# Optimization experiments

Hardware: AMD Instinct MI355X
Metric: run time of the kernel (lower is better)

The kernel has to match this reference:

```python
import jax, jax.numpy as jnp
import numpy as np

NUM_HEADS = 12
EPS = 1e-12  # torch F.normalize clamp_min eps


def _l2norm(t):
    return t / jnp.clip(jnp.linalg.norm(t, axis=-1, keepdims=True), EPS)


def setup_inputs() -> dict:
    key = jax.random.key(0)
    ks = jax.random.split(key, 6)
    B, N, C = 8, 4096, 768
    Nc, Nb, F = 1, 512, 16
    s = 0.02
    return {
        "x": jax.random.normal(ks[0], (B, N, C), jnp.float32),
        "bank": jax.random.normal(ks[1], (Nc, Nb, F), jnp.float32),
        "Wq": jax.random.normal(ks[2], (C, C), jnp.float32) * s,
        "Wkv": jax.random.normal(ks[3], (F, 2 * C), jnp.float32) * s,
        "Wlin": jax.random.normal(ks[4], (C, C), jnp.float32) * s,
        "b_lin": jnp.zeros((C,), jnp.float32),
        "prelu_a": jnp.asarray(0.25, jnp.float32),
        "temperature": jnp.ones((NUM_HEADS, 1, 1), jnp.float32),
    }


def reference(x, bank, Wq, Wkv, Wlin, b_lin, prelu_a, temperature):
    B, N, C = x.shape
    Nc, Nb, _ = bank.shape
    H = NUM_HEADS
    d = C // H
    # q: (B, H, N, d), L2-normalized along d
    q = _l2norm((x @ Wq).reshape(B, N, H, d).transpose(0, 2, 1, 3))
    # kv from (detached) bank: (2, Nc, H, Nb, d)
    kv = (bank @ Wkv).reshape(Nc, Nb, 2, H, d).transpose(2, 0, 3, 1, 4)
    k = _l2norm(kv[0])
    v = kv[1]
    # cosine attention with per-head learned temperature: (B, Nc, H, N, Nb)
    attn = jnp.einsum('bhnd,chmd->bchnm', q, k) * temperature
    attn = jax.nn.softmax(attn, axis=-1)
    # (dropout is identity in eval mode)
    out = jnp.einsum('bchnm,chmd->bchnd', attn, v)  # (B, Nc, H, N, d)
    out = out.reshape(B * Nc, H, N, d).transpose(0, 2, 1, 3).reshape(B, N, C)
    out = out @ Wlin + b_lin
    # PReLU with a single shared parameter
    return jnp.where(out >= 0, out, prelu_a * out)
```

## Files before the change

kernel.cpp:

```cpp
#include <hip/hip_runtime.h>
#include <cstdint>
#include <cstddef>

typedef unsigned short u16;
typedef __attribute__((ext_vector_type(8))) __bf16 bf16x8;
typedef __attribute__((ext_vector_type(4))) float f32x4;

#define MFMA(a, b, c) __builtin_amdgcn_mfma_f32_16x16x32_bf16(a, b, c, 0, 0, 0)

__device__ __forceinline__ u16 f2bf(float f) {
  union { float f; uint32_t u; } x; x.f = f;
  uint32_t r = x.u + 0x7fffu + ((x.u >> 16) & 1u);
  return (u16)(r >> 16);
}

__device__ __forceinline__ void gld16(const u16* g, u16* l) {
  __builtin_amdgcn_global_load_lds(
      (const __attribute__((address_space(1))) void*)g,
      (__attribute__((address_space(3))) void*)l, 16, 0, 0);
}

__global__ void cvt_f32_bf16(const float* __restrict__ src, u16* __restrict__ dst, int n4) {
  int i = blockIdx.x * blockDim.x + threadIdx.x;
  int stride = gridDim.x * blockDim.x;
  for (; i < n4; i += stride) {
    float4 v = ((const float4*)src)[i];
    ushort4 o;
    o.x = f2bf(v.x); o.y = f2bf(v.y); o.z = f2bf(v.z); o.w = f2bf(v.w);
    ((ushort4*)dst)[i] = o;
  }
}

__global__ void prep_kern(const float* __restrict__ Wq, u16* __restrict__ wqt,
                          const float* __restrict__ Wlin, u16* __restrict__ wlt,
                          const float* __restrict__ bank, const float* __restrict__ Wkv,
                          const float* __restrict__ temp, u16* __restrict__ Kb,
                          u16* __restrict__ VT) {
  const int b = blockIdx.x;
  if (b < 1152) {
    __shared__ float tile[32][33];
    const float* src = (b >= 576) ? Wlin : Wq;
    u16* dst = (b >= 576) ? wlt : wqt;
    const int r = (b >= 576) ? b - 576 : b;
    const int bx = (r % 24) * 32, by = (r / 24) * 32;
    const int tx = threadIdx.x & 31, ty = threadIdx.x >> 5;
    #pragma unroll
    for (int i = ty; i < 32; i += 8)
      tile[i][tx] = src[(size_t)(by + i) * 768 + bx + tx];
    __syncthreads();
    #pragma unroll
    for (int i = ty; i < 32; i += 8)
      dst[(size_t)(bx + i) * 768 + by + tx] = f2bf(tile[tx][i]);
  } else {
    const int bb = b - 1152;
    const int h = bb >> 7;
    const int m = ((bb & 127) << 2) + (threadIdx.x >> 6);
    const int j = threadIdx.x & 63;
    const float* br = bank + m * 16;
    float kj = 0.f, vj = 0.f;
    #pragma unroll
    for (int f = 0; f < 16; ++f) {
      float bv = br[f];
      kj = fmaf(bv, Wkv[f * 1536 + h * 64 + j], kj);
      vj = fmaf(bv, Wkv[f * 1536 + 768 + h * 64 + j], vj);
    }
    float ss = kj * kj;
    #pragma unroll
    for (int o = 32; o; o >>= 1) ss += __shfl_xor(ss, o);
    float rn = rsqrtf(fmaxf(ss, 1e-24f));
    Kb[((size_t)h * 512 + m) * 64 + j] = f2bf(kj * rn * temp[h] * 1.4426950408889634f);
    VT[((size_t)h * 64 + j) * 512 + m] = f2bf(vj);
  }
}

template <int MODE>
__global__ __launch_bounds__(256, 3) void gemm_bt(
    const u16* __restrict__ A, const u16* __restrict__ BT, void* __restrict__ Cout,
    int M, int N, int K, const float* __restrict__ bias, const float* __restrict__ prelu) {
  __shared__ u16 sA[3][128 * 32];
  __shared__ u16 sB[3][128 * 32];
  const int ntiles = N >> 7;
  const int swz = (blockIdx.x & 7) * (gridDim.x >> 3) + (blockIdx.x >> 3);
  const int m0 = (swz / ntiles) << 7;
  const int n0 = (swz % ntiles) << 7;
  const int tid = threadIdx.x;
  const int w = tid >> 6, lane = tid & 63;
  const int wm = (w >> 1) << 6, wn = (w & 1) << 6;
  const int srow = lane >> 2, scol = (lane & 3) << 3;
  const u16* ga = A + (size_t)(m0 + (w << 5) + srow) * K + scol;
  const u16* gb = BT + (size_t)(n0 + (w << 5) + srow) * K + scol;
  const int lofs = (w << 5) * 32;
  const int fr = lane & 15, fq = (lane >> 4) << 3;
  f32x4 acc[4][4] = {};

  auto stage = [&](int buf, int k0) {
    gld16(ga + k0, sA[buf] + lofs);
    gld16(ga + k0 + (size_t)16 * K, sA[buf] + lofs + 16 * 32);
    gld16(gb + k0, sB[buf] + lofs);
    gld16(gb + k0 + (size_t)16 * K, sB[buf] + lofs + 16 * 32);
  };

  const int nk = K >> 5;
  stage(0, 0);
  stage(1, 32);
  int cb = 0;
  int sb = 2;
  for (int it = 0; it < nk; ++it) {
    asm volatile("s_waitcnt vmcnt(4)\n\ts_barrier" ::: "memory");
    int nx = it + 2; if (nx >= nk) nx -= nk;
    stage(sb, nx << 5);
    bf16x8 af[4], bfr[4];
    #pragma unroll
    for (int t = 0; t < 4; ++t) {
      af[t] = *(const bf16x8*)(sA[cb] + (wm + t * 16 + fr) * 32 + fq);
      bfr[t] = *(const bf16x8*)(sB[cb] + (wn + t * 16 + fr) * 32 + fq);
    }
    #pragma unroll
    for (int i = 0; i < 4; ++i)
      #pragma unroll
      for (int j = 0; j < 4; ++j)
        acc[i][j] = MFMA(af[i], bfr[j], acc[i][j]);
    cb = (cb == 2) ? 0 : cb + 1;
    sb = (sb == 2) ? 0 : sb + 1;
  }

  const int q = lane >> 4;
  float a = (MODE == 1) ? prelu[0] : 0.f;
  #pragma unroll
  for (int tm = 0; tm < 4; ++tm)
    #pragma unroll
    for (int tn = 0; tn < 4; ++tn) {
      int col = n0 + wn + tn * 16 + fr;
      float bv = (MODE == 1) ? bias[col] : 0.f;
      #pragma unroll
      for (int r = 0; r < 4; ++r) {
        int row = m0 + wm + tm * 16 + q * 4 + r;
        float v = acc[tm][tn][r];
        if (MODE == 1) {
          v += bv;
          v = v >= 0.f ? v : v * a;
          ((float*)Cout)[(size_t)row * N + col] = v;
        } else {
          ((u16*)Cout)[(size_t)row * N + col] = f2bf(v);
        }
      }
    }
}

__global__ __launch_bounds__(512, 4) void attn_kern(
    const u16* __restrict__ Q, const u16* __restrict__ Kb,
    const u16* __restrict__ Vt, u16* __restrict__ O) {
  __shared__ __align__(16) u16 sK[2][64 * 72];
  __shared__ __align__(16) u16 sV[2][64 * 72];

  const int qb = blockIdx.x & 127;
  const int h = blockIdx.x >> 7;
  const int tid = threadIdx.x, w = tid >> 6, lane = tid & 63;
  const int fr = lane & 15, quad = lane >> 4;
  const int rowbase = qb * 256 + (w << 5);

  bf16x8 qa[2][2];
  #pragma unroll
  for (int g = 0; g < 2; ++g) {
    const u16* qp = Q + (size_t)(rowbase + g * 16 + fr) * 768 + h * 64 + (quad << 3);
    qa[g][0] = *(const bf16x8*)qp;
    qa[g][1] = *(const bf16x8*)(qp + 32);
    float ss = 0.f;
    #pragma unroll
    for (int j = 0; j < 8; ++j) {
      float f0 = (float)qa[g][0][j], f1 = (float)qa[g][1][j];
      ss += f0 * f0 + f1 * f1;
    }
    ss += __shfl_xor(ss, 16);
    ss += __shfl_xor(ss, 32);
    float rn = rsqrtf(fmaxf(ss, 1e-24f));
    #pragma unroll
    for (int j = 0; j < 8; ++j) {
      qa[g][0][j] = (__bf16)((float)qa[g][0][j] * rn);
      qa[g][1][j] = (__bf16)((float)qa[g][1][j] * rn);
    }
  }

  const u16* kg = Kb + (size_t)h * 512 * 64;
  const u16* vg = Vt + (size_t)h * 64 * 512;
  int4 kreg, vreg;
  auto load_chunk = [&](int c) {
    kreg = *(const int4*)(kg + (size_t)(c * 64 + (tid >> 3)) * 64 + (tid & 7) * 8);
    vreg = *(const int4*)(vg + (size_t)(tid >> 3) * 512 + c * 64 + (tid & 7) * 8);
  };
  auto store_chunk = [&](int buf) {
    *(int4*)(sK[buf] + (tid >> 3) * 72 + (tid & 7) * 8) = kreg;
    *(int4*)(sV[buf] + (tid >> 3) * 72 + (tid & 7) * 8) = vreg;
  };

  load_chunk(0);
  store_chunk(0);
  load_chunk(1);
  __syncthreads();

  f32x4 oa[2][4] = {};
  f32x4 lsv[2] = {};

  for (int c = 0; c < 8; ++c) {
    const int cb = c & 1;
    if (c < 7) store_chunk((c + 1) & 1);
    if (c < 6) load_chunk(c + 2);

    #pragma unroll
    for (int ks = 0; ks < 2; ++ks) {
      f32x4 s[2][2];
      #pragma unroll
      for (int half = 0; half < 2; ++half) {
        const int mt = ks * 2 + half;
        const u16* kp = sK[cb] + (mt * 16 + fr) * 72 + (quad << 3);
        bf16x8 ak0 = *(const bf16x8*)kp;
        bf16x8 ak1 = *(const bf16x8*)(kp + 32);
        #pragma unroll
        for (int g = 0; g < 2; ++g) {
          f32x4 z = {0.f, 0.f, 0.f, 0.f};
          z = MFMA(ak0, qa[g][0], z);
          z = MFMA(ak1, qa[g][1], z);
          s[g][half] = z;
        }
      }
      bf16x8 pbf[2];
      #pragma unroll
      for (int g = 0; g < 2; ++g)
        #pragma unroll
        for (int half = 0; half < 2; ++half) {
          f32x4 pv;
          #pragma unroll
          for (int r = 0; r < 4; ++r) {
            pv[r] = __builtin_amdgcn_exp2f(s[g][half][r]);
            pbf[g][half * 4 + r] = (__bf16)pv[r];
          }
          lsv[g] += pv;
        }
      #pragma unroll
      for (int t = 0; t < 4; ++t) {
        const u16* vp = sV[cb] + (t * 16 + fr) * 72 + ks * 32 + (quad << 2);
        bf16x8 va;
        *(uint2*)&va = *(const uint2*)vp;
        *((uint2*)&va + 1) = *(const uint2*)(vp + 16);
        #pragma unroll
        for (int g = 0; g < 2; ++g)
          oa[g][t] = MFMA(va, pbf[g], oa[g][t]);
      }
    }
    __syncthreads();
  }

  #pragma unroll
  for (int g = 0; g < 2; ++g) {
    float l = lsv[g][0] + lsv[g][1] + lsv[g][2] + lsv[g][3];
    l += __shfl_xor(l, 16);
    l += __shfl_xor(l, 32);
    float rl = __builtin_amdgcn_rcpf(l);
    u16* op = O + (size_t)(rowbase + g * 16 + fr) * 768 + h * 64 + (quad << 2);
    #pragma unroll
    for (int t = 0; t < 4; ++t) {
      ushort4 pk;
      pk.x = f2bf(oa[g][t][0] * rl);
      pk.y = f2bf(oa[g][t][1] * rl);
      pk.z = f2bf(oa[g][t][2] * rl);
      pk.w = f2bf(oa[g][t][3] * rl);
      *(ushort4*)(op + t * 16) = pk;
    }
  }
}

extern "C" void kernel_launch(void* const* d_in, const int* in_sizes, int n_in,
                              void* d_out, int out_size, void* d_ws, size_t ws_size,
                              hipStream_t stream) {
  const float* x      = (const float*)d_in[0];
  const float* bank   = (const float*)d_in[1];
  const float* Wq     = (const float*)d_in[2];
  const float* Wkv    = (const float*)d_in[3];
  const float* Wlin   = (const float*)d_in[4];
  const float* b_lin  = (const float*)d_in[5];
  const float* prelu  = (const float*)d_in[6];
  const float* temp   = (const float*)d_in[7];
  float* out = (float*)d_out;

  char* ws = (char*)d_ws;
  const size_t NELEM = 25165824;
  u16* qbuf  = (u16*)ws;
  u16* xbuf  = (u16*)(ws + 50331648);
  u16* obuf  = xbuf;
  u16* wqt   = (u16*)(ws + 100663296);
  u16* wlt   = wqt + 589824;
  u16* kbuf  = wlt + 589824;
  u16* vtbuf = kbuf + 393216;

  prep_kern<<<2688, 256, 0, stream>>>(Wq, wqt, Wlin, wlt, bank, Wkv, temp, kbuf, vtbuf);
  cvt_f32_bf16<<<4096, 256, 0, stream>>>(x, xbuf, (int)(NELEM / 4));
  gemm_bt<0><<<1536, 256, 0, stream>>>(xbuf, wqt, qbuf, 32768, 768, 768, nullptr, nullptr);
  attn_kern<<<1536, 512, 0, stream>>>(qbuf, kbuf, vtbuf, obuf);
  gemm_bt<1><<<1536, 256, 0, stream>>>(obuf, wlt, out, 32768, 768, 768, b_lin, prelu);
}
```

Baseline: 356.2 us.

## Shrink attention tiles to 64 query rows per 256-thread block

Measured after the change: 533.9 us. +49.9%, slower.

```diff
diff --git a/kernel.cpp b/kernel.cpp
--- a/kernel.cpp
+++ b/kernel.cpp
@@ -147,28 +147,27 @@
     }
 }
 
-__global__ __launch_bounds__(512, 4) void attn_kern(
+__global__ __launch_bounds__(256, 4) void attn_kern(
     const u16* __restrict__ Q, const u16* __restrict__ Kb,
     const u16* __restrict__ Vt, u16* __restrict__ O) {
   __shared__ __align__(16) u16 sK[2][64 * 72];
   __shared__ __align__(16) u16 sV[2][64 * 72];
 
-  const int qb = blockIdx.x & 127;
-  const int h = blockIdx.x >> 7;
+  const int qb = blockIdx.x & 511;
+  const int h = blockIdx.x >> 9;
   const int tid = threadIdx.x, w = tid >> 6, lane = tid & 63;
   const int fr = lane & 15, quad = lane >> 4;
-  const int rowbase = qb * 256 + (w << 5);
-
-  bf16x8 qa[2][2];
-  #pragma unroll
-  for (int g = 0; g < 2; ++g) {
-    const u16* qp = Q + (size_t)(rowbase + g * 16 + fr) * 768 + h * 64 + (quad << 3);
-    qa[g][0] = *(const bf16x8*)qp;
-    qa[g][1] = *(const bf16x8*)(qp + 32);
+  const int row0 = qb * 64 + (w << 4) + fr;
+
+  bf16x8 qa0, qa1;
+  {
+    const u16* qp = Q + (size_t)row0 * 768 + h * 64 + (quad << 3);
+    qa0 = *(const bf16x8*)qp;
+    qa1 = *(const bf16x8*)(qp + 32);
     float ss = 0.f;
     #pragma unroll
     for (int j = 0; j < 8; ++j) {
-      float f0 = (float)qa[g][0][j], f1 = (float)qa[g][1][j];
+      float f0 = (float)qa0[j], f1 = (float)qa1[j];
       ss += f0 * f0 + f1 * f1;
     }
     ss += __shfl_xor(ss, 16);
@@ -176,21 +175,29 @@
     float rn = rsqrtf(fmaxf(ss, 1e-24f));
     #pragma unroll
     for (int j = 0; j < 8; ++j) {
-      qa[g][0][j] = (__bf16)((float)qa[g][0][j] * rn);
-      qa[g][1][j] = (__bf16)((float)qa[g][1][j] * rn);
+      qa0[j] = (__bf16)((float)qa0[j] * rn);
+      qa1[j] = (__bf16)((float)qa1[j] * rn);
     }
   }
 
   const u16* kg = Kb + (size_t)h * 512 * 64;
   const u16* vg = Vt + (size_t)h * 64 * 512;
-  int4 kreg, vreg;
+  int4 kreg[2], vreg[2];
   auto load_chunk = [&](int c) {
-    kreg = *(const int4*)(kg + (size_t)(c * 64 + (tid >> 3)) * 64 + (tid & 7) * 8);
-    vreg = *(const int4*)(vg + (size_t)(tid >> 3) * 512 + c * 64 + (tid & 7) * 8);
+    #pragma unroll
+    for (int r = 0; r < 2; ++r) {
+      int u = r * 256 + tid;
+      kreg[r] = *(const int4*)(kg + (size_t)(c * 64 + (u >> 3)) * 64 + (u & 7) * 8);
+      vreg[r] = *(const int4*)(vg + (size_t)(u >> 3) * 512 + c * 64 + (u & 7) * 8);
+    }
   };
   auto store_chunk = [&](int buf) {
-    *(int4*)(sK[buf] + (tid >> 3) * 72 + (tid & 7) * 8) = kreg;
-    *(int4*)(sV[buf] + (tid >> 3) * 72 + (tid & 7) * 8) = vreg;
+    #pragma unroll
+    for (int r = 0; r < 2; ++r) {
+      int u = r * 256 + tid;
+      *(int4*)(sK[buf] + (u >> 3) * 72 + (u & 7) * 8) = kreg[r];
+      *(int4*)(sV[buf] + (u >> 3) * 72 + (u & 7) * 8) = vreg[r];
+    }
   };
 
   load_chunk(0);
@@ -198,72 +205,64 @@
   load_chunk(1);
   __syncthreads();
 
-  f32x4 oa[2][4] = {};
-  f32x4 lsv[2] = {};
+  f32x4 oa[4] = {};
+  f32x4 lsv = {};
 
   for (int c = 0; c < 8; ++c) {
-    const int cb = c & 1;
+    const int cbuf = c & 1;
     if (c < 7) store_chunk((c + 1) & 1);
     if (c < 6) load_chunk(c + 2);
 
     #pragma unroll
     for (int ks = 0; ks < 2; ++ks) {
-      f32x4 s[2][2];
+      f32x4 s[2];
       #pragma unroll
       for (int half = 0; half < 2; ++half) {
         const int mt = ks * 2 + half;
-        const u16* kp = sK[cb] + (mt * 16 + fr) * 72 + (quad << 3);
+        const u16* kp = sK[cbuf] + (mt * 16 + fr) * 72 + (quad << 3);
         bf16x8 ak0 = *(const bf16x8*)kp;
         bf16x8 ak1 = *(const bf16x8*)(kp + 32);
+        f32x4 z = {0.f, 0.f, 0.f, 0.f};
+        z = MFMA(ak0, qa0, z);
+        z = MFMA(ak1, qa1, z);
+        s[half] = z;
+      }
+      bf16x8 pbf;
+      #pragma unroll
+      for (int half = 0; half < 2; ++half) {
+        f32x4 pv;
         #pragma unroll
-        for (int g = 0; g < 2; ++g) {
-          f32x4 z = {0.f, 0.f, 0.f, 0.f};
-          z = MFMA(ak0, qa[g][0], z);
-          z = MFMA(ak1, qa[g][1], z);
-          s[g][half] = z;
+        for (int r = 0; r < 4; ++r) {
+          pv[r] = __builtin_amdgcn_exp2f(s[half][r]);
+          pbf[half * 4 + r] = (__bf16)pv[r];
         }
-      }
-      bf16x8 pbf[2];
-      #pragma unroll
-      for (int g = 0; g < 2; ++g)
-        #pragma unroll
-        for (int half = 0; half < 2; ++half) {
-          f32x4 pv;
-          #pragma unroll
-          for (int r = 0; r < 4; ++r) {
-            pv[r] = __builtin_amdgcn_exp2f(s[g][half][r]);
-            pbf[g][half * 4 + r] = (__bf16)pv[r];
-          }
-          lsv[g] += pv;
-        }
+        lsv += pv;
+      }
       #pragma unroll
       for (int t = 0; t < 4; ++t) {
-        const u16* vp = sV[cb] + (t * 16 + fr) * 72 + ks * 32 + (quad << 2);
+        const u16* vp = sV[cbuf] + (t * 16 + fr) * 72 + ks * 32 + (quad << 2);
         bf16x8 va;
         *(uint2*)&va = *(const uint2*)vp;
         *((uint2*)&va + 1) = *(const uint2*)(vp + 16);
-        #pragma unroll
-        for (int g = 0; g < 2; ++g)
-          oa[g][t] = MFMA(va, pbf[g], oa[g][t]);
+        oa[t] = MFMA(va, pbf, oa[t]);
       }
     }
     __syncthreads();
   }
 
-  #pragma unroll
-  for (int g = 0; g < 2; ++g) {
-    float l = lsv[g][0] + lsv[g][1] + lsv[g][2] + lsv[g][3];
+  {
+    float l = lsv[0] + lsv[1] + lsv[2] + lsv[3];
     l += __shfl_xor(l, 16);
     l += __shfl_xor(l, 32);
     float rl = __builtin_amdgcn_rcpf(l);
-    u16* op = O + (size_t)(rowbase + g * 16 + fr) * 768 + h * 64 + (quad << 2);
+    u16* op = O + (size_t)row0 * 768 + h * 64 + (quad << 2);
     #pragma unroll
     for (int t = 0; t < 4; ++t) {
       ushort4 pk;
-      pk.x = f2bf(oa[g][t][0] * rl);
-      pk.y = f2bf(oa[g][t][1] * rl);
-      pk.z = f2bf(oa[g][t][2] * rl);
-      pk.w = f2bf(oa[g][t][3] * rl);
+      pk.x = f2bf(oa[t][0] * rl);
+      pk.y = f2bf(oa[t][1] * rl);
+      pk.z = f2bf(oa[t][2] * rl);
+      pk.w = f2bf(oa[t][3] * rl);
       *(ushort4*)(op + t * 16) = pk;
     }
   }
@@ -295,6 +294,6 @@
   prep_kern<<<2688, 256, 0, stream>>>(Wq, wqt, Wlin, wlt, bank, Wkv, temp, kbuf, vtbuf);
   cvt_f32_bf16<<<4096, 256, 0, stream>>>(x, xbuf, (int)(NELEM / 4));
   gemm_bt<0><<<1536, 256, 0, stream>>>(xbuf, wqt, qbuf, 32768, 768, 768, nullptr, nullptr);
-  attn_kern<<<1536, 512, 0, stream>>>(qbuf, kbuf, vtbuf, obuf);
+  attn_kern<<<6144, 256, 0, stream>>>(qbuf, kbuf, vtbuf, obuf);
   gemm_bt<1><<<1536, 256, 0, stream>>>(obuf, wlt, out, 32768, 768, 768, b_lin, prelu);
 }
```

## Fuse fp32-to-bf16 conversion of x into Q projection GEMM loads

Applied to the files above, without the earlier changes.

After: 372.6 us. +4.6%, slower.

```diff
diff --git a/kernel.cpp b/kernel.cpp
--- a/kernel.cpp
+++ b/kernel.cpp
@@ -14,21 +14,15 @@
   return (u16)(r >> 16);
 }
 
+__device__ __forceinline__ u16 bfbits(float f) {
+  __bf16 b = (__bf16)f;
+  return *(u16*)&b;
+}
+
 __device__ __forceinline__ void gld16(const u16* g, u16* l) {
   __builtin_amdgcn_global_load_lds(
       (const __attribute__((address_space(1))) void*)g,
       (__attribute__((address_space(3))) void*)l, 16, 0, 0);
-}
-
-__global__ void cvt_f32_bf16(const float* __restrict__ src, u16* __restrict__ dst, int n4) {
-  int i = blockIdx.x * blockDim.x + threadIdx.x;
-  int stride = gridDim.x * blockDim.x;
-  for (; i < n4; i += stride) {
-    float4 v = ((const float4*)src)[i];
-    ushort4 o;
-    o.x = f2bf(v.x); o.y = f2bf(v.y); o.z = f2bf(v.z); o.w = f2bf(v.w);
-    ((ushort4*)dst)[i] = o;
-  }
 }
 
 __global__ void prep_kern(const float* __restrict__ Wq, u16* __restrict__ wqt,
@@ -75,7 +69,7 @@
 
 template <int MODE>
 __global__ __launch_bounds__(256, 3) void gemm_bt(
-    const u16* __restrict__ A, const u16* __restrict__ BT, void* __restrict__ Cout,
+    const void* __restrict__ Ain, const u16* __restrict__ BT, void* __restrict__ Cout,
     int M, int N, int K, const float* __restrict__ bias, const float* __restrict__ prelu) {
   __shared__ u16 sA[3][128 * 32];
   __shared__ u16 sB[3][128 * 32];
@@ -87,28 +81,17 @@
   const int w = tid >> 6, lane = tid & 63;
   const int wm = (w >> 1) << 6, wn = (w & 1) << 6;
   const int srow = lane >> 2, scol = (lane & 3) << 3;
-  const u16* ga = A + (size_t)(m0 + (w << 5) + srow) * K + scol;
   const u16* gb = BT + (size_t)(n0 + (w << 5) + srow) * K + scol;
   const int lofs = (w << 5) * 32;
   const int fr = lane & 15, fq = (lane >> 4) << 3;
   f32x4 acc[4][4] = {};
-
-  auto stage = [&](int buf, int k0) {
-    gld16(ga + k0, sA[buf] + lofs);
-    gld16(ga + k0 + (size_t)16 * K, sA[buf] + lofs + 16 * 32);
+  const int nk = K >> 5;
+
+  auto loadB = [&](int buf, int k0) {
     gld16(gb + k0, sB[buf] + lofs);
     gld16(gb + k0 + (size_t)16 * K, sB[buf] + lofs + 16 * 32);
   };
-
-  const int nk = K >> 5;
-  stage(0, 0);
-  stage(1, 32);
-  int cb = 0;
-  int sb = 2;
-  for (int it = 0; it < nk; ++it) {
-    asm volatile("s_waitcnt vmcnt(4)\n\ts_barrier" ::: "memory");
-    int nx = it + 2; if (nx >= nk) nx -= nk;
-    stage(sb, nx << 5);
+  auto compute = [&](int cb) {
     bf16x8 af[4], bfr[4];
     #pragma unroll
     for (int t = 0; t < 4; ++t) {
@@ -120,8 +103,65 @@
       #pragma unroll
       for (int j = 0; j < 4; ++j)
         acc[i][j] = MFMA(af[i], bfr[j], acc[i][j]);
-    cb = (cb == 2) ? 0 : cb + 1;
-    sb = (sb == 2) ? 0 : sb + 1;
+  };
+
+  if (MODE == 1) {
+    const u16* ga = (const u16*)Ain + (size_t)(m0 + (w << 5) + srow) * K + scol;
+    auto stage = [&](int buf, int k0) {
+      gld16(ga + k0, sA[buf] + lofs);
+      gld16(ga + k0 + (size_t)16 * K, sA[buf] + lofs + 16 * 32);
+      loadB(buf, k0);
+    };
+    stage(0, 0);
+    stage(1, 32);
+    int cb = 0, sb = 2;
+    for (int it = 0; it < nk; ++it) {
+      asm volatile("s_waitcnt vmcnt(4)\n\ts_barrier" ::: "memory");
+      int nx = it + 2; if (nx >= nk) nx -= nk;
+      stage(sb, nx << 5);
+      compute(cb);
+      cb = (cb == 2) ? 0 : cb + 1;
+      sb = (sb == 2) ? 0 : sb + 1;
+    }
+  } else {
+    const float* gaf = (const float*)Ain;
+    float4 ra[4], rb[4];
+    auto loadA = [&](float4 (&rg)[4], int k0) {
+      #pragma unroll
+      for (int g = 0; g < 4; ++g) {
+        int u = g * 256 + tid;
+        rg[g] = *(const float4*)(gaf + (size_t)(m0 + (u >> 3)) * K + k0 + (u & 7) * 4);
+      }
+    };
+    auto writeA = [&](float4 (&rg)[4], int buf) {
+      #pragma unroll
+      for (int g = 0; g < 4; ++g) {
+        int u = g * 256 + tid;
+        float4 v = rg[g];
+        ushort4 pk = { bfbits(v.x), bfbits(v.y), bfbits(v.z), bfbits(v.w) };
+        *(ushort4*)(sA[buf] + (u >> 3) * 32 + (u & 7) * 4) = pk;
+      }
+    };
+    loadA(ra, 0);
+    loadB(0, 0);
+    asm volatile("s_waitcnt vmcnt(2)" ::: "memory");
+    writeA(ra, 0);
+    loadA(rb, 32);
+    loadB(1, 32);
+    auto iter = [&](int it, float4 (&wrA)[4], float4 (&ldA)[4]) {
+      asm volatile("s_waitcnt vmcnt(2) lgkmcnt(0)\n\ts_barrier" ::: "memory");
+      int wb = it + 1; wb -= (wb >= 3) ? 3 : 0;
+      while (wb >= 3) wb -= 3;
+      writeA(wrA, wb);
+      int nx = it + 2; if (nx >= nk) nx -= nk;
+      loadA(ldA, nx << 5);
+      loadB((it + 2) % 3, nx << 5);
+      compute(it % 3);
+    };
+    for (int it = 0; it < nk; it += 2) {
+      iter(it, rb, ra);
+      iter(it + 1, ra, rb);
+    }
   }
 
   const int q = lane >> 4;
@@ -283,18 +323,15 @@
   float* out = (float*)d_out;
 
   char* ws = (char*)d_ws;
-  const size_t NELEM = 25165824;
   u16* qbuf  = (u16*)ws;
-  u16* xbuf  = (u16*)(ws + 50331648);
-  u16* obuf  = xbuf;
+  u16* obuf  = (u16*)(ws + 50331648);
   u16* wqt   = (u16*)(ws + 100663296);
   u16* wlt   = wqt + 589824;
   u16* kbuf  = wlt + 589824;
   u16* vtbuf = kbuf + 393216;
 
   prep_kern<<<2688, 256, 0, stream>>>(Wq, wqt, Wlin, wlt, bank, Wkv, temp, kbuf, vtbuf);
-  cvt_f32_bf16<<<4096, 256, 0, stream>>>(x, xbuf, (int)(NELEM / 4));
-  gemm_bt<0><<<1536, 256, 0, stream>>>(xbuf, wqt, qbuf, 32768, 768, 768, nullptr, nullptr);
+  gemm_bt<0><<<1536, 256, 0, stream>>>(x, wqt, qbuf, 32768, 768, 768, nullptr, nullptr);
   attn_kern<<<1536, 512, 0, stream>>>(qbuf, kbuf, vtbuf, obuf);
   gemm_bt<1><<<1536, 256, 0, stream>>>(obuf, wlt, out, 32768, 768, 768, b_lin, prelu);
 }
```
